# Optimization experiments

Hardware: AMD Instinct MI355X
Metric: run time of the kernel (lower is better)

## Reference

```python
import jax, jax.numpy as jnp
import numpy as np

NUM_CLASSES = 81
NEG_POS_RATIO = 3  # neg_pos init arg
POS_FRAC = 0.02    # realistic fraction of matched (positive) priors


def setup_inputs() -> dict:
    key = jax.random.key(0)
    k1, k2, k3, k4, k5 = jax.random.split(key, 5)
    B, P, C = 32, 24564, NUM_CLASSES
    loc_data = jax.random.normal(k1, (B, P, 4), jnp.float32)
    conf_data = jax.random.normal(k2, (B, P, C), jnp.float32)
    loc_targets = jax.random.normal(k3, (B, P, 4), jnp.float32)
    raw_labels = jax.random.randint(k4, (B, P), 1, C)
    is_pos = jax.random.uniform(k5, (B, P)) < POS_FRAC
    conf_targets = jnp.where(is_pos, raw_labels, 0).astype(jnp.int32)
    return {"loc_data": loc_data, "conf_data": conf_data,
            "loc_targets": loc_targets, "conf_targets": conf_targets}


def _smooth_l1(x):
    ax = jnp.abs(x)
    return jnp.where(ax < 1.0, 0.5 * x * x, ax - 0.5)


def reference(loc_data, conf_data, loc_targets, conf_targets):
    # loc_data [B,P,4], conf_data [B,P,C], conf_targets [B,P] int
    B, P, C = conf_data.shape
    pos = conf_targets > 0  # [B,P]

    # localization smooth-L1 over positive priors only (sum reduction)
    loc_loss = jnp.sum(_smooth_l1(loc_data - loc_targets) * pos[..., None].astype(loc_data.dtype))

    # per-prior CE loss: logsumexp - logit[target]
    lse = jax.nn.logsumexp(conf_data, axis=-1)  # [B,P]
    tgt_logit = jnp.take_along_axis(conf_data, conf_targets[..., None].astype(jnp.int32), axis=-1)[..., 0]
    ce = lse - tgt_logit  # [B,P]

    # hard negative mining: zero out positives, sort descending, pick pivot at 3*num_pos
    mined = jnp.where(pos, 0.0, ce)
    sorted_desc = jnp.flip(jnp.sort(mined, axis=1), axis=1)  # [B,P]
    num_pos = jnp.sum(pos, axis=1)  # [B]
    num_neg = jnp.clip(NEG_POS_RATIO * num_pos, 0, P - 1)
    pivot = jnp.take_along_axis(sorted_desc, num_neg[:, None], axis=1)  # [B,1]
    neg = mined > pivot

    sel = (pos | neg).astype(ce.dtype)
    conf_loss = jnp.sum(ce * sel)

    n_matched = jnp.maximum(jnp.sum(num_pos), 1).astype(conf_data.dtype)
    return (loc_loss + conf_loss) / n_matched
```

## Files before the change

### kernel.cpp

```cpp
#include <hip/hip_runtime.h>
#include <cmath>
#include <cstdint>

#define NB 32
#define NP 24564
#define NC 81
#define NEG_POS 3

static constexpr size_t MINED_ELEMS = (size_t)NB * NP;
static constexpr size_t MINED_BYTES = MINED_ELEMS * sizeof(float);

#define NTILES4 ((int)(MINED_ELEMS / 4))
#define MAIN_BLOCKS 2047
#define TOTAL_WAVES (MAIN_BLOCKS * 4)
#define ITERS 24


__device__ __forceinline__ float wave_reduce_sum(float v) {
#pragma unroll
  for (int off = 32; off > 0; off >>= 1) v += __shfl_down(v, off, 64);
  return v;
}

__device__ __forceinline__ float smooth_l1_4(float4 a, float4 t) {
  float acc = 0.f, d, ax;
  d = a.x - t.x; ax = fabsf(d); acc += (ax < 1.f) ? 0.5f * d * d : ax - 0.5f;
  d = a.y - t.y; ax = fabsf(d); acc += (ax < 1.f) ? 0.5f * d * d : ax - 0.5f;
  d = a.z - t.z; ax = fabsf(d); acc += (ax < 1.f) ? 0.5f * d * d : ax - 0.5f;
  d = a.w - t.w; ax = fabsf(d); acc += (ax < 1.f) ? 0.5f * d * d : ax - 0.5f;
  return acc;
}

__global__ void mb_init(double* __restrict__ acc, int* __restrict__ num_pos) {
  int t = threadIdx.x;
  if (t < 3) acc[t] = 0.0;
  if (t < NB) num_pos[t] = 0;
}

__global__ __launch_bounds__(256, 8) void mb_main(
    const float* __restrict__ conf_data, const int* __restrict__ conf_targets,
    float* __restrict__ mined) {
  __shared__ float lds[4][332];

  const int tid  = (int)threadIdx.x;
  const int wid  = tid >> 6, lane = tid & 63;
  const int r    = lane >> 4, il = lane & 15;
  float* __restrict__ L = lds[wid];

  const int l17   = (lane < 17) ? lane : 16;
  const int ldst1 = (lane < 17) ? (256 + 4 * l17) : 328;

  int tile = (int)blockIdx.x * 4 + wid;
  float4 c0, c1;
  int4 tgCur, tgN;
  {
    const float4* __restrict__ src =
        reinterpret_cast<const float4*>(conf_data) + (size_t)tile * 81;
    c0 = src[lane];
    c1 = src[64 + l17];
    tgCur = *reinterpret_cast<const int4*>(conf_targets + (size_t)tile * 4);
  }

#pragma unroll 1
  for (int k = 0; k < ITERS; ++k) {
    *reinterpret_cast<float4*>(&L[4 * lane]) = c0;
    *reinterpret_cast<float4*>(&L[ldst1]) = c1;

    {
      int nt = tile + TOTAL_WAVES;
      nt = (nt < NTILES4) ? nt : tile;
      const float4* __restrict__ src =
          reinterpret_cast<const float4*>(conf_data) + (size_t)nt * 81;
      c0 = src[lane];
      c1 = src[64 + l17];
      tgN = *reinterpret_cast<const int4*>(conf_targets + (size_t)nt * 4);
    }
    __builtin_amdgcn_sched_barrier(0);

    const int tgt = (r == 0) ? tgCur.x : (r == 1) ? tgCur.y
                  : (r == 2) ? tgCur.z : tgCur.w;

    const int rb = 81 * r;
    float e = __expf(L[rb + il]) + __expf(L[rb + il + 16]) +
              __expf(L[rb + il + 32]) + __expf(L[rb + il + 48]) +
              __expf(L[rb + il + 64]);
    if (il == 0) e += __expf(L[rb + 80]);
    e += __shfl_xor(e, 1, 64);
    e += __shfl_xor(e, 2, 64);
    e += __shfl_xor(e, 4, 64);
    e += __shfl_xor(e, 8, 64);

    const float tv = L[rb + tgt];
    const float ce = __logf(e) - tv;
    const float val = (tgt > 0) ? -ce : ce;
    mined[tile * 4 + r] = val;

    tgCur = tgN;
    tile += TOTAL_WAVES;
  }
}

__global__ __launch_bounds__(1024) void mb_select(
    const float* __restrict__ mined, const float* __restrict__ loc_data,
    const float* __restrict__ loc_targets, double* __restrict__ acc,
    int* __restrict__ num_pos) {
  const int b = blockIdx.x;
  const float* __restrict__ row = mined + (size_t)b * NP;
  const int tid = threadIdx.x;
  const int wid = tid >> 6;
  const int lane = tid & 63;

  __shared__ int hist[16][256];
  __shared__ int total[256];
  __shared__ int suffix[256];
  __shared__ unsigned s_prefix;
  __shared__ int s_k;

  {
    int np = 0;
    float cp = 0.f, lv = 0.f;
    for (int q = tid; q < NP / 4; q += 1024) {
      const float4 v = reinterpret_cast<const float4*>(row)[q];
      const float vv[4] = {v.x, v.y, v.z, v.w};
#pragma unroll
      for (int j = 0; j < 4; ++j) {
        if (__float_as_uint(vv[j]) >> 31) {
          np++;
          cp += -vv[j];
          const size_t flat = (size_t)b * NP + 4 * q + j;
          lv += smooth_l1_4(
              *reinterpret_cast<const float4*>(loc_data + flat * 4),
              *reinterpret_cast<const float4*>(loc_targets + flat * 4));
        }
      }
    }
    __shared__ float rednp[16], redcp[16], redlv[16];
    float wnp = wave_reduce_sum((float)np);
    float wcp = wave_reduce_sum(cp);
    float wlv = wave_reduce_sum(lv);
    if (lane == 0) { rednp[wid] = wnp; redcp[wid] = wcp; redlv[wid] = wlv; }
    __syncthreads();
    if (tid == 0) {
      float tnp = 0.f, tcp = 0.f, tlv = 0.f;
#pragma unroll
      for (int i = 0; i < 16; ++i) { tnp += rednp[i]; tcp += redcp[i]; tlv += redlv[i]; }
      const int npi = (int)tnp;
      num_pos[b] = npi;
      if (tcp != 0.f) atomicAdd(&acc[1], (double)tcp);
      if (tlv != 0.f) atomicAdd(&acc[0], (double)tlv);
      int k = NEG_POS * npi;
      if (k > NP - 1) k = NP - 1;
      s_k = k;
      s_prefix = 0u;
    }
    __syncthreads();
  }

  for (int shift = 24; shift >= 0; shift -= 8) {
    for (int i = tid; i < 16 * 256; i += 1024) ((int*)hist)[i] = 0;
    __syncthreads();
    const unsigned mask = (shift == 24) ? 0u : (0xFFFFFFFFu << (shift + 8));
    const unsigned pfx = s_prefix;
    const int kcur = s_k;

    for (int q = tid; q < NP / 4; q += 1024) {
      const float4 v = reinterpret_cast<const float4*>(row)[q];
      unsigned u;
      u = __float_as_uint(v.x); u = (u >> 31) ? 0u : u; if ((u & mask) == pfx) atomicAdd(&hist[wid][(u >> shift) & 255], 1);
      u = __float_as_uint(v.y); u = (u >> 31) ? 0u : u; if ((u & mask) == pfx) atomicAdd(&hist[wid][(u >> shift) & 255], 1);
      u = __float_as_uint(v.z); u = (u >> 31) ? 0u : u; if ((u & mask) == pfx) atomicAdd(&hist[wid][(u >> shift) & 255], 1);
      u = __float_as_uint(v.w); u = (u >> 31) ? 0u : u; if ((u & mask) == pfx) atomicAdd(&hist[wid][(u >> shift) & 255], 1);
    }
    __syncthreads();

    if (tid < 256) {
      int t = 0;
#pragma unroll
      for (int w = 0; w < 16; ++w) t += hist[w][tid];
      total[tid] = t;
    }
    __syncthreads();

    if (wid == 0) {
      const int t0_ = total[4 * lane + 0];
      const int t1_ = total[4 * lane + 1];
      const int t2_ = total[4 * lane + 2];
      const int t3_ = total[4 * lane + 3];
      const int s3 = t3_;
      const int s2 = t2_ + s3;
      const int s1 = t1_ + s2;
      const int s0 = t0_ + s1;
      int acc_ = s0;
#pragma unroll
      for (int off = 1; off < 64; off <<= 1) {
        const int o = __shfl_down(acc_, off, 64);
        if (lane + off < 64) acc_ += o;
      }
      const int excl = acc_ - s0;
      suffix[4 * lane + 0] = s0 + excl;
      suffix[4 * lane + 1] = s1 + excl;
      suffix[4 * lane + 2] = s2 + excl;
      suffix[4 * lane + 3] = s3 + excl;
    }
    __syncthreads();

    if (tid < 256) {
      const int cs = suffix[tid] - total[tid];
      if (kcur >= cs && kcur < cs + total[tid]) {
        s_prefix = pfx | ((unsigned)tid << shift);
        s_k = kcur - cs;
      }
    }
    __syncthreads();
  }

  const unsigned vbits = s_prefix;
  float sum = 0.f;
  for (int q = tid; q < NP / 4; q += 1024) {
    const float4 v = reinterpret_cast<const float4*>(row)[q];
    unsigned u;
    u = __float_as_uint(v.x); u = (u >> 31) ? 0u : u; if (u > vbits) sum += v.x;
    u = __float_as_uint(v.y); u = (u >> 31) ? 0u : u; if (u > vbits) sum += v.y;
    u = __float_as_uint(v.z); u = (u >> 31) ? 0u : u; if (u > vbits) sum += v.z;
    u = __float_as_uint(v.w); u = (u >> 31) ? 0u : u; if (u > vbits) sum += v.w;
  }

  __shared__ float wsum[16];
  float w = wave_reduce_sum(sum);
  if (lane == 0) wsum[wid] = w;
  __syncthreads();
  if (tid == 0) {
    float t = 0.f;
#pragma unroll
    for (int i = 0; i < 16; ++i) t += wsum[i];
    atomicAdd(&acc[2], (double)t);
  }
}

__global__ void mb_finalize(const double* __restrict__ acc,
                            const int* __restrict__ num_pos,
                            float* __restrict__ out) {
  if (threadIdx.x == 0) {
    int tot = 0;
#pragma unroll
    for (int i = 0; i < NB; ++i) tot += num_pos[i];
    const double n = (double)(tot > 0 ? tot : 1);
    out[0] = (float)((acc[0] + acc[1] + acc[2]) / n);
  }
}

extern "C" void kernel_launch(void* const* d_in, const int* in_sizes, int n_in,
                              void* d_out, int out_size, void* d_ws, size_t ws_size,
                              hipStream_t stream) {
  const float* loc_data     = (const float*)d_in[0];
  const float* conf_data    = (const float*)d_in[1];
  const float* loc_targets  = (const float*)d_in[2];
  const int*   conf_targets = (const int*)d_in[3];
  float* out = (float*)d_out;

  float*  mined   = (float*)d_ws;
  double* acc     = (double*)((char*)d_ws + MINED_BYTES);
  int*    num_pos = (int*)((char*)d_ws + MINED_BYTES + 3 * sizeof(double));

  mb_init<<<1, 64, 0, stream>>>(acc, num_pos);

  mb_main<<<MAIN_BLOCKS, 256, 0, stream>>>(conf_data, conf_targets, mined);

  mb_select<<<NB, 1024, 0, stream>>>(mined, loc_data, loc_targets, acc, num_pos);

  mb_finalize<<<1, 64, 0, stream>>>(acc, num_pos, out);
}
```

Baseline: 99.46 us.

## Double-buffer conf tile prefetch and replace atomic accumulation with per-block partials

```diff
diff --git a/kernel.cpp b/kernel.cpp
--- a/kernel.cpp
+++ b/kernel.cpp
@@ -13,7 +13,7 @@
 #define NTILES4 ((int)(MINED_ELEMS / 4))
 #define MAIN_BLOCKS 2047
 #define TOTAL_WAVES (MAIN_BLOCKS * 4)
-#define ITERS 24
+#define KITERS 12
 
 
 __device__ __forceinline__ float wave_reduce_sum(float v) {
@@ -31,12 +31,6 @@
   return acc;
 }
 
-__global__ void mb_init(double* __restrict__ acc, int* __restrict__ num_pos) {
-  int t = threadIdx.x;
-  if (t < 3) acc[t] = 0.0;
-  if (t < NB) num_pos[t] = 0;
-}
-
 __global__ __launch_bounds__(256, 8) void mb_main(
     const float* __restrict__ conf_data, const int* __restrict__ conf_targets,
     float* __restrict__ mined) {
@@ -50,59 +44,85 @@
   const int l17   = (lane < 17) ? lane : 16;
   const int ldst1 = (lane < 17) ? (256 + 4 * l17) : 328;
 
+#define LOAD_DATA(c0, c1, t)                                            \
+  do {                                                                  \
+    const float4* __restrict__ _s =                                     \
+        reinterpret_cast<const float4*>(conf_data) + (size_t)(t) * 81;  \
+    (c0) = _s[lane];                                                    \
+    (c1) = _s[64 + l17];                                                \
+  } while (0)
+
+#define STAGE(c0, c1)                                  \
+  do {                                                 \
+    *reinterpret_cast<float4*>(&L[4 * lane]) = (c0);   \
+    *reinterpret_cast<float4*>(&L[ldst1]) = (c1);      \
+  } while (0)
+
+#define COMPUTE(t, tg)                                                  \
+  do {                                                                  \
+    const int tgt = (r == 0) ? (tg).x : (r == 1) ? (tg).y               \
+                  : (r == 2) ? (tg).z : (tg).w;                         \
+    const int rb = 81 * r;                                              \
+    float e = __expf(L[rb + il]) + __expf(L[rb + il + 16]) +            \
+              __expf(L[rb + il + 32]) + __expf(L[rb + il + 48]) +       \
+              __expf(L[rb + il + 64]);                                  \
+    if (il == 0) e += __expf(L[rb + 80]);                               \
+    e += __shfl_xor(e, 1, 64);                                          \
+    e += __shfl_xor(e, 2, 64);                                          \
+    e += __shfl_xor(e, 4, 64);                                          \
+    e += __shfl_xor(e, 8, 64);                                          \
+    const float tv = L[rb + tgt];                                       \
+    const float ce = __logf(e) - tv;                                    \
+    const float val = (tgt > 0) ? -ce : ce;                             \
+    mined[(t) * 4 + r] = val;                                           \
+  } while (0)
+
   int tile = (int)blockIdx.x * 4 + wid;
-  float4 c0, c1;
-  int4 tgCur, tgN;
+  float4 cA0, cA1, cB0, cB1;
+  int4 tg0, tg1, tgN;
+
+  LOAD_DATA(cA0, cA1, tile);
+  tg0 = *reinterpret_cast<const int4*>(conf_targets + (size_t)tile * 4);
   {
-    const float4* __restrict__ src =
-        reinterpret_cast<const float4*>(conf_data) + (size_t)tile * 81;
-    c0 = src[lane];
-    c1 = src[64 + l17];
-    tgCur = *reinterpret_cast<const int4*>(conf_targets + (size_t)tile * 4);
+    const int tB = tile + TOTAL_WAVES;
+    LOAD_DATA(cB0, cB1, tB);
+    tg1 = *reinterpret_cast<const int4*>(conf_targets + (size_t)tB * 4);
   }
 
 #pragma unroll 1
-  for (int k = 0; k < ITERS; ++k) {
-    *reinterpret_cast<float4*>(&L[4 * lane]) = c0;
-    *reinterpret_cast<float4*>(&L[ldst1]) = c1;
-
+  for (int k = 0; k < KITERS; ++k) {
+    STAGE(cA0, cA1);
     {
-      int nt = tile + TOTAL_WAVES;
+      int nt = tile + 2 * TOTAL_WAVES;
       nt = (nt < NTILES4) ? nt : tile;
-      const float4* __restrict__ src =
-          reinterpret_cast<const float4*>(conf_data) + (size_t)nt * 81;
-      c0 = src[lane];
-      c1 = src[64 + l17];
+      LOAD_DATA(cA0, cA1, nt);
       tgN = *reinterpret_cast<const int4*>(conf_targets + (size_t)nt * 4);
     }
     __builtin_amdgcn_sched_barrier(0);
-
-    const int tgt = (r == 0) ? tgCur.x : (r == 1) ? tgCur.y
-                  : (r == 2) ? tgCur.z : tgCur.w;
-
-    const int rb = 81 * r;
-    float e = __expf(L[rb + il]) + __expf(L[rb + il + 16]) +
-              __expf(L[rb + il + 32]) + __expf(L[rb + il + 48]) +
-              __expf(L[rb + il + 64]);
-    if (il == 0) e += __expf(L[rb + 80]);
-    e += __shfl_xor(e, 1, 64);
-    e += __shfl_xor(e, 2, 64);
-    e += __shfl_xor(e, 4, 64);
-    e += __shfl_xor(e, 8, 64);
-
-    const float tv = L[rb + tgt];
-    const float ce = __logf(e) - tv;
-    const float val = (tgt > 0) ? -ce : ce;
-    mined[tile * 4 + r] = val;
-
-    tgCur = tgN;
+    COMPUTE(tile, tg0);
+    tg0 = tg1; tg1 = tgN;
     tile += TOTAL_WAVES;
-  }
+
+    STAGE(cB0, cB1);
+    {
+      int nt = tile + 2 * TOTAL_WAVES;
+      nt = (nt < NTILES4) ? nt : tile;
+      LOAD_DATA(cB0, cB1, nt);
+      tgN = *reinterpret_cast<const int4*>(conf_targets + (size_t)nt * 4);
+    }
+    __builtin_amdgcn_sched_barrier(0);
+    COMPUTE(tile, tg0);
+    tg0 = tg1; tg1 = tgN;
+    tile += TOTAL_WAVES;
+  }
+#undef LOAD_DATA
+#undef STAGE
+#undef COMPUTE
 }
 
 __global__ __launch_bounds__(1024) void mb_select(
     const float* __restrict__ mined, const float* __restrict__ loc_data,
-    const float* __restrict__ loc_targets, double* __restrict__ acc,
+    const float* __restrict__ loc_targets, float* __restrict__ partial,
     int* __restrict__ num_pos) {
   const int b = blockIdx.x;
   const float* __restrict__ row = mined + (size_t)b * NP;
@@ -146,8 +166,8 @@
       for (int i = 0; i < 16; ++i) { tnp += rednp[i]; tcp += redcp[i]; tlv += redlv[i]; }
       const int npi = (int)tnp;
       num_pos[b] = npi;
-      if (tcp != 0.f) atomicAdd(&acc[1], (double)tcp);
-      if (tlv != 0.f) atomicAdd(&acc[0], (double)tlv);
+      partial[b * 4 + 0] = tlv;
+      partial[b * 4 + 1] = tcp;
       int k = NEG_POS * npi;
       if (k > NP - 1) k = NP - 1;
       s_k = k;
@@ -233,19 +253,24 @@
     float t = 0.f;
 #pragma unroll
     for (int i = 0; i < 16; ++i) t += wsum[i];
-    atomicAdd(&acc[2], (double)t);
-  }
-}
-
-__global__ void mb_finalize(const double* __restrict__ acc,
+    partial[b * 4 + 2] = t;
+  }
+}
+
+__global__ void mb_finalize(const float* __restrict__ partial,
                             const int* __restrict__ num_pos,
                             float* __restrict__ out) {
   if (threadIdx.x == 0) {
+    double s = 0.0;
     int tot = 0;
 #pragma unroll
-    for (int i = 0; i < NB; ++i) tot += num_pos[i];
+    for (int i = 0; i < NB; ++i) {
+      s += (double)partial[i * 4 + 0] + (double)partial[i * 4 + 1] +
+           (double)partial[i * 4 + 2];
+      tot += num_pos[i];
+    }
     const double n = (double)(tot > 0 ? tot : 1);
-    out[0] = (float)((acc[0] + acc[1] + acc[2]) / n);
+    out[0] = (float)(s / n);
   }
 }
 
@@ -258,15 +283,13 @@
   const int*   conf_targets = (const int*)d_in[3];
   float* out = (float*)d_out;
 
-  float*  mined   = (float*)d_ws;
-  double* acc     = (double*)((char*)d_ws + MINED_BYTES);
-  int*    num_pos = (int*)((char*)d_ws + MINED_BYTES + 3 * sizeof(double));
-
-  mb_init<<<1, 64, 0, stream>>>(acc, num_pos);
+  float* mined   = (float*)d_ws;
+  float* partial = (float*)((char*)d_ws + MINED_BYTES);
+  int*   num_pos = (int*)((char*)d_ws + MINED_BYTES + 512);
 
   mb_main<<<MAIN_BLOCKS, 256, 0, stream>>>(conf_data, conf_targets, mined);
 
-  mb_select<<<NB, 1024, 0, stream>>>(mined, loc_data, loc_targets, acc, num_pos);
-
-  mb_finalize<<<1, 64, 0, stream>>>(acc, num_pos, out);
-}
+  mb_select<<<NB, 1024, 0, stream>>>(mined, loc_data, loc_targets, partial, num_pos);
+
+  mb_finalize<<<1, 64, 0, stream>>>(partial, num_pos, out);
+}
```

New measurement: 95.79 us. -3.7%, faster.
